# Kernel optimization log

Hardware: AMD Instinct MI355X
Metric: run time of the kernel (lower is better)

The kernel has to match this reference:

```python
import jax, jax.numpy as jnp
import numpy as np

B, L, F, R = 32, 128, 128, 4096
MAX_INTERIOR = R >> 1  # tpr.max_interior_index
N = 262144


def setup_inputs() -> dict:
    key = jax.random.key(0)
    ks = jax.random.split(key, 7)
    mem_values = jax.random.normal(ks[0], (N, F), dtype=jnp.float32)
    # zero out a slice of rows so the ConsNet pad_mask path is exercised
    mem_values = mem_values.at[: N // 20].set(0.0)
    arg_weights = jax.random.uniform(ks[1], (B, L, 4), dtype=jnp.float32)
    root_filler = jax.random.normal(ks[2], (B, F), dtype=jnp.float32)
    op_dist = jax.random.uniform(ks[3], (B, 3), dtype=jnp.float32)
    batch_idx = jax.random.randint(ks[4], (N,), 0, B, dtype=jnp.int32)
    slot_idx = jax.random.randint(ks[5], (N,), 0, L, dtype=jnp.int32)
    role_idx = jax.random.randint(ks[6], (N,), 0, R, dtype=jnp.int32)
    return {
        "mem_values": mem_values,
        "arg_weights": arg_weights,
        "root_filler": root_filler,
        "op_dist": op_dist,
        "batch_idx": batch_idx,
        "slot_idx": slot_idx,
        "role_idx": role_idx,
    }


def _forward(mem_values, arg_weights, root_filler, op_dist,
             batch_idx, slot_idx, role_idx):
    # per-entry gather of the 4 argument weights: w[n,k] = arg_weights[b_n, l_n, k]
    w = arg_weights[batch_idx, slot_idx]  # [N, 4]
    flat = batch_idx.astype(jnp.int32) * R + role_idx  # [N], coalesce key (b, r)

    def coalesce(vals):  # scatter-add == torch_sparse.coalesce into dense [B,R,F]
        g = jnp.zeros((B * R, F), vals.dtype).at[flat].add(vals)
        return g.reshape(B, R, F)

    H = R >> 1

    # ---- CarNet (sparse): weight, coalesce, keep even roles, role >>= 1 ----
    car_A = coalesce(mem_values * w[:, 0:1])            # [B,R,F]
    car_out = jnp.zeros((B, R, F), mem_values.dtype).at[:, :H].set(car_A[:, 0::2])

    # ---- CdrNet (sparse): keep odd roles != 1, role >>= 1 ----
    cdr_A = coalesce(mem_values * w[:, 1:2])
    cdr_half = cdr_A[:, 1::2]                            # roles 2r+1 -> r
    cdr_half = cdr_half.at[:, 0].set(0.0)                # exclude old role 1 (r=0)
    cdr_out = jnp.zeros((B, R, F), mem_values.dtype).at[:, :H].set(cdr_half)

    # ---- ConsNet (sparse): pad-mask weights, roles<MAX_INTERIOR, children + root ----
    pad = jnp.all(mem_values == 0, axis=1, keepdims=True)  # [N,1]
    c1 = coalesce(mem_values * jnp.where(pad, 0.0, w[:, 2:3]))
    c2 = coalesce(mem_values * jnp.where(pad, 0.0, w[:, 3:4]))
    cons_out = jnp.zeros((B, R, F), mem_values.dtype)
    cons_out = cons_out.at[:, 0::2].set(c1[:, :MAX_INTERIOR])      # r -> 2r
    cons_out = cons_out.at[:, 1::2].add(c2[:, :MAX_INTERIOR])      # r -> 2r+1
    cons_out = cons_out.at[:, 1].add(root_filler)                  # root at role 1

    # ---- op-distribution weighted combine (coalesce of the 3 streams) ----
    out = (op_dist[:, 0, None, None] * car_out
           + op_dist[:, 1, None, None] * cdr_out
           + op_dist[:, 2, None, None] * cons_out)
    return out


def reference(mem_values, arg_weights, root_filler, op_dist,
              batch_idx, slot_idx, role_idx):
    return _forward(mem_values, arg_weights, root_filler, op_dist,
                    batch_idx, slot_idx, role_idx)
```

## Files before the change

### kernel.cpp

```cpp
#include <hip/hip_runtime.h>


namespace {
constexpr int kB = 32;
constexpr int kL = 128;
constexpr int kF = 128;
constexpr int kR = 4096;
constexpr int kN = 262144;
constexpr int kNB = kB * kR;
constexpr int kCap = 32;
constexpr int kOvfMax = 4096;

constexpr size_t kOffCounts = 0;
constexpr size_t kOffOvfCnt = (size_t)kNB * 4;
constexpr size_t kOffOvf    = kOffOvfCnt + 16;
constexpr size_t kOffTokW   = 544768;
constexpr size_t kOffBuck   = kOffTokW + (size_t)kN * 16;
}

__global__ __launch_bounds__(256) void build_kernel(
    const float4* __restrict__ aw, const float* __restrict__ opd,
    const int* __restrict__ bidx, const int* __restrict__ sidx,
    const int* __restrict__ ridx,
    int* __restrict__ counts, int* __restrict__ ovf_cnt,
    int* __restrict__ ovf, float4* __restrict__ tokw,
    int* __restrict__ buckets) {
  int n = blockIdx.x * 256 + threadIdx.x;
  if (n >= kN) return;
  int b = bidx[n];
  int s = sidx[n];
  int rr = ridx[n];
  float4 w = aw[b * kL + s];
  float op0 = opd[3 * b + 0];
  float op1 = opd[3 * b + 1];
  float op2 = opd[3 * b + 2];
  float4 pw;
  pw.x = w.x * op0;
  pw.y = w.y * op1;
  pw.z = w.z * op2;
  pw.w = w.w * op2;
  tokw[n] = pw;
  int key = (b << 12) | rr;
  int pos = atomicAdd(&counts[key], 1);
  if (pos < kCap) {
    buckets[(size_t)key * kCap + pos] = n;
  } else {
    int o = atomicAdd(ovf_cnt, 1);
    if (o < kOvfMax) ovf[o] = n;
  }
}

template <int CH>
__device__ __forceinline__ float pick_scale(float4 w, bool odd) {
  if (CH == 0) return w.x;
  if (CH == 1) return w.y;
  return odd ? w.w : w.z;
}

template <int CH>
__device__ __forceinline__ void proc4(int i0, int cnt, int idxvec, int laneoff,
                                      bool odd,
                                      const float4* __restrict__ tokw,
                                      const float2* __restrict__ mem2, int t,
                                      float& ax, float& ay) {
  int n0 = __shfl(idxvec, laneoff + i0 + 0);
  int n1 = __shfl(idxvec, laneoff + i0 + 1);
  int n2 = __shfl(idxvec, laneoff + i0 + 2);
  int n3 = __shfl(idxvec, laneoff + i0 + 3);
  const bool v0 = (i0 + 0) < cnt, v1 = (i0 + 1) < cnt;
  const bool v2 = (i0 + 2) < cnt, v3 = (i0 + 3) < cnt;
  n0 = v0 ? n0 : 0;
  n1 = v1 ? n1 : 0;
  n2 = v2 ? n2 : 0;
  n3 = v3 ? n3 : 0;
  float4 w0 = tokw[n0], w1 = tokw[n1], w2 = tokw[n2], w3 = tokw[n3];
  float2 m0 = mem2[(size_t)n0 * (kF / 2) + t];
  float2 m1 = mem2[(size_t)n1 * (kF / 2) + t];
  float2 m2 = mem2[(size_t)n2 * (kF / 2) + t];
  float2 m3 = mem2[(size_t)n3 * (kF / 2) + t];
  float s0 = v0 ? pick_scale<CH>(w0, odd) : 0.f;
  float s1 = v1 ? pick_scale<CH>(w1, odd) : 0.f;
  float s2 = v2 ? pick_scale<CH>(w2, odd) : 0.f;
  float s3 = v3 ? pick_scale<CH>(w3, odd) : 0.f;
  ax += s0 * m0.x; ay += s0 * m0.y;
  ax += s1 * m1.x; ay += s1 * m1.y;
  ax += s2 * m2.x; ay += s2 * m2.y;
  ax += s3 * m3.x; ay += s3 * m3.y;
}

__global__ __launch_bounds__(256) void gather_kernel(
    const float2* __restrict__ mem2, const float4* __restrict__ tokw,
    const float2* __restrict__ root2, const float* __restrict__ opd,
    const int* __restrict__ counts, const int* __restrict__ buckets,
    float2* __restrict__ out2) {
  const int row = blockIdx.x * 4 + (threadIdx.x >> 6);
  const int t = threadIdx.x & 63;
  const int ts = t & 31;
  const int b = row >> 12;
  const int r = row & (kR - 1);
  const bool odd = (r & 1) != 0;
  const bool lo = r < (kR / 2);

  const int keyC = (b << 12) | (r >> 1);
  const int keyA = (b << 12) | ((r << 1) & (kR - 1));

  int cntC_raw = counts[keyC];
  int2 cntAD_raw = *(const int2*)(counts + keyA);
  int idxC = buckets[(size_t)keyC * kCap + ts];
  int idxAD = buckets[(size_t)keyA * kCap + t];

  const int cntC = min(cntC_raw, kCap);
  const int cntA = lo ? min(cntAD_raw.x, kCap) : 0;
  const int cntD = (lo && r >= 1) ? min(cntAD_raw.y, kCap) : 0;

  float ax = 0.f, ay = 0.f;

  proc4<2>(0, cntC, idxC, 0, odd, tokw, mem2, t, ax, ay);
  if (lo) {
    proc4<0>(0, cntA, idxAD, 0, odd, tokw, mem2, t, ax, ay);
    proc4<1>(0, cntD, idxAD, 32, odd, tokw, mem2, t, ax, ay);
  }

  for (int i = 4; i < cntC; i += 4)
    proc4<2>(i, cntC, idxC, 0, odd, tokw, mem2, t, ax, ay);
  for (int i = 4; i < cntA; i += 4)
    proc4<0>(i, cntA, idxAD, 0, odd, tokw, mem2, t, ax, ay);
  for (int i = 4; i < cntD; i += 4)
    proc4<1>(i, cntD, idxAD, 32, odd, tokw, mem2, t, ax, ay);

  if (r == 1) {
    float2 rf = root2[b * (kF / 2) + t];
    float op2 = opd[3 * b + 2];
    ax += op2 * rf.x;
    ay += op2 * rf.y;
  }
  float2 o;
  o.x = ax;
  o.y = ay;
  out2[(size_t)row * (kF / 2) + t] = o;
}

__global__ __launch_bounds__(128) void ovf_kernel(
    const float* __restrict__ mem, const float4* __restrict__ tokw,
    const int* __restrict__ bidx, const int* __restrict__ ridx,
    const int* __restrict__ ovf_cnt, const int* __restrict__ ovf,
    float* __restrict__ out) {
  int m = *ovf_cnt;
  if (m > kOvfMax) m = kOvfMax;
  const int t = threadIdx.x;
  for (int i = blockIdx.x; i < m; i += gridDim.x) {
    int n = ovf[i];
    int b = bidx[n];
    int rr = ridx[n];
    float4 w = tokw[n];
    float mv = mem[(size_t)n * kF + t];
    size_t base = ((size_t)b * kR) * kF;
    if ((rr & 1) == 0)
      atomicAdd(&out[base + (size_t)(rr >> 1) * kF + t], w.x * mv);
    if ((rr & 1) && rr >= 3)
      atomicAdd(&out[base + (size_t)((rr - 1) >> 1) * kF + t], w.y * mv);
    if (rr < kR / 2) {
      atomicAdd(&out[base + (size_t)(2 * rr) * kF + t], w.z * mv);
      atomicAdd(&out[base + (size_t)(2 * rr + 1) * kF + t], w.w * mv);
    }
  }
}

extern "C" void kernel_launch(void* const* d_in, const int* in_sizes, int n_in,
                              void* d_out, int out_size, void* d_ws, size_t ws_size,
                              hipStream_t stream) {
  const float* mem   = (const float*)d_in[0];
  const float* aw    = (const float*)d_in[1];
  const float* rootf = (const float*)d_in[2];
  const float* opd   = (const float*)d_in[3];
  const int* bidx    = (const int*)d_in[4];
  const int* sidx    = (const int*)d_in[5];
  const int* ridx    = (const int*)d_in[6];

  char* ws = (char*)d_ws;
  int* counts    = (int*)(ws + kOffCounts);
  int* ovf_cnt   = (int*)(ws + kOffOvfCnt);
  int* ovf       = (int*)(ws + kOffOvf);
  float4* tokw   = (float4*)(ws + kOffTokW);
  int* buckets   = (int*)(ws + kOffBuck);

  hipMemsetAsync(ws, 0, kOffOvfCnt + 4, stream);

  build_kernel<<<kN / 256, 256, 0, stream>>>(
      (const float4*)aw, opd, bidx, sidx, ridx, counts, ovf_cnt, ovf, tokw,
      buckets);

  gather_kernel<<<kNB / 4, 256, 0, stream>>>(
      (const float2*)mem, tokw, (const float2*)rootf, opd, counts, buckets,
      (float2*)d_out);

  ovf_kernel<<<64, 128, 0, stream>>>(
      mem, tokw, bidx, ridx, ovf_cnt, ovf, (float*)d_out);
}
```

Before: 312.6 us.

## Bucket entries by output row with precomputed scale instead of source role

The build kernel now pushes each entry directly into the output-row buckets it contributes to, storing (index, scale) pairs, rather than bucketing by source role and resolving car/cdr/cons mapping at gather time. The gather kernel then reads a single bucket per output row with wave-uniform indices via readfirstlane, dropping the tokw table and the three separate loops. In exchange the build kernel does up to three atomics per entry and writes more bucket data, and the bucket capacity now depends on workspace size, which could send more entries to the atomic overflow path.

```diff
diff --git a/kernel.cpp b/kernel.cpp
--- a/kernel.cpp
+++ b/kernel.cpp
@@ -8,23 +8,21 @@
 constexpr int kR = 4096;
 constexpr int kN = 262144;
 constexpr int kNB = kB * kR;
-constexpr int kCap = 32;
-constexpr int kOvfMax = 4096;
+constexpr int kCapMax = 32;
+constexpr int kOvfMax = 65536;
 
-constexpr size_t kOffCounts = 0;
-constexpr size_t kOffOvfCnt = (size_t)kNB * 4;
-constexpr size_t kOffOvf    = kOffOvfCnt + 16;
-constexpr size_t kOffTokW   = 544768;
-constexpr size_t kOffBuck   = kOffTokW + (size_t)kN * 16;
+constexpr size_t kOffCounts  = 0;
+constexpr size_t kOffOvfCnt  = 524288;
+constexpr size_t kOffOvf     = 524304;
+constexpr size_t kOffEntries = 1572880;
 }
 
 __global__ __launch_bounds__(256) void build_kernel(
     const float4* __restrict__ aw, const float* __restrict__ opd,
     const int* __restrict__ bidx, const int* __restrict__ sidx,
-    const int* __restrict__ ridx,
+    const int* __restrict__ ridx, int cap,
     int* __restrict__ counts, int* __restrict__ ovf_cnt,
-    int* __restrict__ ovf, float4* __restrict__ tokw,
-    int* __restrict__ buckets) {
+    int4* __restrict__ ovf, int2* __restrict__ entries) {
   int n = blockIdx.x * 256 + threadIdx.x;
   if (n >= kN) return;
   int b = bidx[n];
@@ -34,103 +32,80 @@
   float op0 = opd[3 * b + 0];
   float op1 = opd[3 * b + 1];
   float op2 = opd[3 * b + 2];
-  float4 pw;
-  pw.x = w.x * op0;
-  pw.y = w.y * op1;
-  pw.z = w.z * op2;
-  pw.w = w.w * op2;
-  tokw[n] = pw;
-  int key = (b << 12) | rr;
-  int pos = atomicAdd(&counts[key], 1);
-  if (pos < kCap) {
-    buckets[(size_t)key * kCap + pos] = n;
-  } else {
-    int o = atomicAdd(ovf_cnt, 1);
-    if (o < kOvfMax) ovf[o] = n;
+  const int base = b << 12;
+
+  auto push = [&](int row, float sc) {
+    int key = base | row;
+    int pos = atomicAdd(&counts[key], 1);
+    if (pos < cap) {
+      entries[(size_t)key * cap + pos] = make_int2(n, __float_as_int(sc));
+    } else {
+      int o = atomicAdd(ovf_cnt, 1);
+      if (o < kOvfMax) ovf[o] = make_int4(key, n, __float_as_int(sc), 0);
+    }
+  };
+
+  if ((rr & 1) == 0) {
+    push(rr >> 1, op0 * w.x);
+  } else if (rr >= 3) {
+    push((rr - 1) >> 1, op1 * w.y);
+  }
+  if (rr < kR / 2) {
+    push(2 * rr, op2 * w.z);
+    push(2 * rr + 1, op2 * w.w);
   }
 }
 
-template <int CH>
-__device__ __forceinline__ float pick_scale(float4 w, bool odd) {
-  if (CH == 0) return w.x;
-  if (CH == 1) return w.y;
-  return odd ? w.w : w.z;
-}
-
-template <int CH>
-__device__ __forceinline__ void proc4(int i0, int cnt, int idxvec, int laneoff,
-                                      bool odd,
-                                      const float4* __restrict__ tokw,
+__device__ __forceinline__ void proc4(int i0, int cnt, int2 e,
                                       const float2* __restrict__ mem2, int t,
                                       float& ax, float& ay) {
-  int n0 = __shfl(idxvec, laneoff + i0 + 0);
-  int n1 = __shfl(idxvec, laneoff + i0 + 1);
-  int n2 = __shfl(idxvec, laneoff + i0 + 2);
-  int n3 = __shfl(idxvec, laneoff + i0 + 3);
-  const bool v0 = (i0 + 0) < cnt, v1 = (i0 + 1) < cnt;
-  const bool v2 = (i0 + 2) < cnt, v3 = (i0 + 3) < cnt;
-  n0 = v0 ? n0 : 0;
+  int n0 = __builtin_amdgcn_readfirstlane(__shfl(e.x, i0 + 0));
+  int s0 = __builtin_amdgcn_readfirstlane(__shfl(e.y, i0 + 0));
+  int n1 = __builtin_amdgcn_readfirstlane(__shfl(e.x, i0 + 1));
+  int s1 = __builtin_amdgcn_readfirstlane(__shfl(e.y, i0 + 1));
+  int n2 = __builtin_amdgcn_readfirstlane(__shfl(e.x, i0 + 2));
+  int s2 = __builtin_amdgcn_readfirstlane(__shfl(e.y, i0 + 2));
+  int n3 = __builtin_amdgcn_readfirstlane(__shfl(e.x, i0 + 3));
+  int s3 = __builtin_amdgcn_readfirstlane(__shfl(e.y, i0 + 3));
+  const bool v1 = (i0 + 1) < cnt, v2 = (i0 + 2) < cnt, v3 = (i0 + 3) < cnt;
   n1 = v1 ? n1 : 0;
   n2 = v2 ? n2 : 0;
   n3 = v3 ? n3 : 0;
-  float4 w0 = tokw[n0], w1 = tokw[n1], w2 = tokw[n2], w3 = tokw[n3];
+  float f0 = __int_as_float(s0);
+  float f1 = v1 ? __int_as_float(s1) : 0.f;
+  float f2 = v2 ? __int_as_float(s2) : 0.f;
+  float f3 = v3 ? __int_as_float(s3) : 0.f;
   float2 m0 = mem2[(size_t)n0 * (kF / 2) + t];
   float2 m1 = mem2[(size_t)n1 * (kF / 2) + t];
   float2 m2 = mem2[(size_t)n2 * (kF / 2) + t];
   float2 m3 = mem2[(size_t)n3 * (kF / 2) + t];
-  float s0 = v0 ? pick_scale<CH>(w0, odd) : 0.f;
-  float s1 = v1 ? pick_scale<CH>(w1, odd) : 0.f;
-  float s2 = v2 ? pick_scale<CH>(w2, odd) : 0.f;
-  float s3 = v3 ? pick_scale<CH>(w3, odd) : 0.f;
-  ax += s0 * m0.x; ay += s0 * m0.y;
-  ax += s1 * m1.x; ay += s1 * m1.y;
-  ax += s2 * m2.x; ay += s2 * m2.y;
-  ax += s3 * m3.x; ay += s3 * m3.y;
+  ax += f0 * m0.x; ay += f0 * m0.y;
+  ax += f1 * m1.x; ay += f1 * m1.y;
+  ax += f2 * m2.x; ay += f2 * m2.y;
+  ax += f3 * m3.x; ay += f3 * m3.y;
 }
 
 __global__ __launch_bounds__(256) void gather_kernel(
-    const float2* __restrict__ mem2, const float4* __restrict__ tokw,
-    const float2* __restrict__ root2, const float* __restrict__ opd,
-    const int* __restrict__ counts, const int* __restrict__ buckets,
-    float2* __restrict__ out2) {
+    const float2* __restrict__ mem2, const float2* __restrict__ root2,
+    const float* __restrict__ opd, const int* __restrict__ counts,
+    const int2* __restrict__ entries, int cap, float2* __restrict__ out2) {
   const int row = blockIdx.x * 4 + (threadIdx.x >> 6);
   const int t = threadIdx.x & 63;
-  const int ts = t & 31;
-  const int b = row >> 12;
-  const int r = row & (kR - 1);
-  const bool odd = (r & 1) != 0;
-  const bool lo = r < (kR / 2);
-
-  const int keyC = (b << 12) | (r >> 1);
-  const int keyA = (b << 12) | ((r << 1) & (kR - 1));
-
-  int cntC_raw = counts[keyC];
-  int2 cntAD_raw = *(const int2*)(counts + keyA);
-  int idxC = buckets[(size_t)keyC * kCap + ts];
-  int idxAD = buckets[(size_t)keyA * kCap + t];
-
-  const int cntC = min(cntC_raw, kCap);
-  const int cntA = lo ? min(cntAD_raw.x, kCap) : 0;
-  const int cntD = (lo && r >= 1) ? min(cntAD_raw.y, kCap) : 0;
+  int cnt = min(counts[row], cap);
+  cnt = __builtin_amdgcn_readfirstlane(cnt);
 
   float ax = 0.f, ay = 0.f;
-
-  proc4<2>(0, cntC, idxC, 0, odd, tokw, mem2, t, ax, ay);
-  if (lo) {
-    proc4<0>(0, cntA, idxAD, 0, odd, tokw, mem2, t, ax, ay);
-    proc4<1>(0, cntD, idxAD, 32, odd, tokw, mem2, t, ax, ay);
+  if (cnt > 0) {
+    int2 e = make_int2(0, 0);
+    if (t < cnt) e = entries[(size_t)row * cap + t];
+    for (int i = 0; i < cnt; i += 4) proc4(i, cnt, e, mem2, t, ax, ay);
   }
 
-  for (int i = 4; i < cntC; i += 4)
-    proc4<2>(i, cntC, idxC, 0, odd, tokw, mem2, t, ax, ay);
-  for (int i = 4; i < cntA; i += 4)
-    proc4<0>(i, cntA, idxAD, 0, odd, tokw, mem2, t, ax, ay);
-  for (int i = 4; i < cntD; i += 4)
-    proc4<1>(i, cntD, idxAD, 32, odd, tokw, mem2, t, ax, ay);
-
+  const int r = row & (kR - 1);
   if (r == 1) {
+    const int b = row >> 12;
+    float op2 = opd[3 * b + 2];
     float2 rf = root2[b * (kF / 2) + t];
-    float op2 = opd[3 * b + 2];
     ax += op2 * rf.x;
     ay += op2 * rf.y;
   }
@@ -141,28 +116,15 @@
 }
 
 __global__ __launch_bounds__(128) void ovf_kernel(
-    const float* __restrict__ mem, const float4* __restrict__ tokw,
-    const int* __restrict__ bidx, const int* __restrict__ ridx,
-    const int* __restrict__ ovf_cnt, const int* __restrict__ ovf,
-    float* __restrict__ out) {
+    const float* __restrict__ mem, const int* __restrict__ ovf_cnt,
+    const int4* __restrict__ ovf, float* __restrict__ out) {
   int m = *ovf_cnt;
   if (m > kOvfMax) m = kOvfMax;
   const int t = threadIdx.x;
   for (int i = blockIdx.x; i < m; i += gridDim.x) {
-    int n = ovf[i];
-    int b = bidx[n];
-    int rr = ridx[n];
-    float4 w = tokw[n];
-    float mv = mem[(size_t)n * kF + t];
-    size_t base = ((size_t)b * kR) * kF;
-    if ((rr & 1) == 0)
-      atomicAdd(&out[base + (size_t)(rr >> 1) * kF + t], w.x * mv);
-    if ((rr & 1) && rr >= 3)
-      atomicAdd(&out[base + (size_t)((rr - 1) >> 1) * kF + t], w.y * mv);
-    if (rr < kR / 2) {
-      atomicAdd(&out[base + (size_t)(2 * rr) * kF + t], w.z * mv);
-      atomicAdd(&out[base + (size_t)(2 * rr + 1) * kF + t], w.w * mv);
-    }
+    int4 e = ovf[i];
+    float sc = __int_as_float(e.z);
+    atomicAdd(&out[(size_t)e.x * kF + t], sc * mem[(size_t)e.y * kF + t]);
   }
 }
 
@@ -180,20 +142,26 @@
   char* ws = (char*)d_ws;
   int* counts    = (int*)(ws + kOffCounts);
   int* ovf_cnt   = (int*)(ws + kOffOvfCnt);
-  int* ovf       = (int*)(ws + kOffOvf);
-  float4* tokw   = (float4*)(ws + kOffTokW);
-  int* buckets   = (int*)(ws + kOffBuck);
+  int4* ovf      = (int4*)(ws + kOffOvf);
+  int2* entries  = (int2*)(ws + kOffEntries);
+
+  int cap = kCapMax;
+  if (ws_size > kOffEntries) {
+    size_t avail = (ws_size - kOffEntries) / ((size_t)kNB * sizeof(int2));
+    if (avail < (size_t)cap) cap = (int)avail;
+  } else {
+    cap = 0;
+  }
 
   hipMemsetAsync(ws, 0, kOffOvfCnt + 4, stream);
 
   build_kernel<<<kN / 256, 256, 0, stream>>>(
-      (const float4*)aw, opd, bidx, sidx, ridx, counts, ovf_cnt, ovf, tokw,
-      buckets);
+      (const float4*)aw, opd, bidx, sidx, ridx, cap, counts, ovf_cnt, ovf,
+      entries);
 
   gather_kernel<<<kNB / 4, 256, 0, stream>>>(
-      (const float2*)mem, tokw, (const float2*)rootf, opd, counts, buckets,
+      (const float2*)mem, (const float2*)rootf, opd, counts, entries, cap,
       (float2*)d_out);
 
-  ovf_kernel<<<64, 128, 0, stream>>>(
-      mem, tokw, bidx, ridx, ovf_cnt, ovf, (float*)d_out);
+  ovf_kernel<<<64, 128, 0, stream>>>(mem, ovf_cnt, ovf, (float*)d_out);
 }
```

Result: faster. 299.5 us (-4.2%).
